# Performance work log

Hardware: AMD Instinct MI355X
Metric: run time of the kernel (lower is better)

The kernel has to match this reference:

```python
import jax, jax.numpy as jnp
import numpy as np

B, S, D = 2, 2048, 1024
H, DH, DM = 16, 64, 4096
EPS = 1e-5
IGNORE = -100000.0


def setup_inputs() -> dict:
    key = jax.random.key(0)
    ks = jax.random.split(key, 14)
    s = 0.02
    return {
        "x": jax.random.normal(ks[0], (B, S, D), jnp.float32),
        "W_Q": jax.random.normal(ks[1], (H, DH, D), jnp.float32) * s,
        "W_K": jax.random.normal(ks[2], (H, DH, D), jnp.float32) * s,
        "W_V": jax.random.normal(ks[3], (H, DH, D), jnp.float32) * s,
        "W_O": jax.random.normal(ks[4], (H, D, DH), jnp.float32) * s,
        "b_Q": jax.random.normal(ks[5], (H, DH), jnp.float32) * s,
        "b_K": jax.random.normal(ks[6], (H, DH), jnp.float32) * s,
        "b_V": jax.random.normal(ks[7], (H, DH), jnp.float32) * s,
        "b_O": jax.random.normal(ks[8], (D,), jnp.float32) * s,
        "W_in": jax.random.normal(ks[9], (DM, D), jnp.float32) * s,
        "b_in": jax.random.normal(ks[10], (DM,), jnp.float32) * s,
        "W_out": jax.random.normal(ks[11], (D, DM), jnp.float32) * s,
        "b_out": jax.random.normal(ks[12], (D,), jnp.float32) * s,
    }


def ln_pre(x):
    x = x - jnp.mean(x, axis=-1, keepdims=True)
    scale = jnp.sqrt(jnp.mean(x * x, axis=-1, keepdims=True) + EPS)
    return x / scale


def gelu_new(x):
    c = np.sqrt(2.0 / np.pi).astype(np.float32)
    return 0.5 * x * (1.0 + jnp.tanh(c * (x + 0.044715 * x ** 3)))


def reference(x, W_Q, W_K, W_V, W_O, b_Q, b_K, b_V, b_O, W_in, b_in, W_out, b_out):
    resid_pre = x
    xn = ln_pre(resid_pre)
    # q,k,v: [B, S, H, DH]
    q = jnp.einsum('ihm,bpm->bpih', W_Q, xn) + b_Q
    k = jnp.einsum('ihm,bpm->bpih', W_K, xn) + b_K
    v = jnp.einsum('ihm,bpm->bpih', W_V, xn) + b_V
    attn_scale = np.sqrt(DH).astype(np.float32)
    # scores: [B, H, Sq, Sk]  (einsum 'bpih,bqih->bipq')
    scores = jnp.einsum('bpih,bqih->bipq', q, k) / attn_scale
    mask = jnp.tril(jnp.ones((S, S), bool))
    scores = jnp.where(mask, scores, IGNORE)
    attn = jax.nn.softmax(scores, axis=-1)
    # z: [B, Sq, H, DH]
    z = jnp.einsum('bpih,biqp->bqih', v, attn)
    attn_out = jnp.einsum('idh,bqih->bqd', W_O, z) + b_O
    resid_mid = resid_pre + attn_out
    m = ln_pre(resid_mid)
    pre = jnp.einsum('md,bpd->bpm', W_in, m) + b_in
    post = gelu_new(pre)
    mlp_out = jnp.einsum('dm,bpm->bpd', W_out, post) + b_out
    return resid_mid + mlp_out
```

## Files before the change

### kernel.cpp

```cpp
#include <hip/hip_runtime.h>

typedef unsigned short u16;
typedef __attribute__((ext_vector_type(8))) short short8;
typedef __attribute__((ext_vector_type(4))) unsigned short ushort4v;
typedef __attribute__((ext_vector_type(4))) float float4v;

__device__ __forceinline__ float bf2f(u16 u) {
  union { unsigned int i; float f; } c; c.i = ((unsigned int)u) << 16; return c.f;
}
__device__ __forceinline__ u16 f2bf(float f) {
  union { float f; unsigned int i; } c; c.f = f;
  unsigned int u = c.i;
  return (u16)((u + 0x7fffu + ((u >> 16) & 1u)) >> 16);
}
__device__ __forceinline__ float gelu_new(float x) {
  const float k1 = 2.30218776f;
  const float k3 = 0.10294233f;
  float x3 = x * x * x;
  float e = __builtin_amdgcn_exp2f(-(k1 * x + k3 * x3));
  return x / (1.0f + e);
}
__device__ __forceinline__ float ldres(const float* p) { return *p; }
__device__ __forceinline__ float ldres(const u16* p) { return bf2f(*p); }

__device__ __forceinline__ void gload_lds16(const u16* g, u16* l) {
  __builtin_amdgcn_global_load_lds(
      (const __attribute__((address_space(1))) unsigned int*)g,
      (__attribute__((address_space(3))) unsigned int*)l, 16, 0, 0);
}

__global__ void cvt_bf16(const float* __restrict__ src, u16* __restrict__ dst) {
  int t = blockIdx.x * 256 + threadIdx.x;
  float4v a = *(const float4v*)(src + (size_t)t * 8);
  float4v b = *(const float4v*)(src + (size_t)t * 8 + 4);
  short8 o;
#pragma unroll
  for (int j = 0; j < 4; ++j) o[j] = (short)f2bf(a[j]);
#pragma unroll
  for (int j = 0; j < 4; ++j) o[4 + j] = (short)f2bf(b[j]);
  *(short8*)(dst + (size_t)t * 8) = o;
}

__global__ void prep_wo(const float* __restrict__ WO, u16* __restrict__ Wot) {
  int t = blockIdx.x * 256 + threadIdx.x;
  int i = t >> 13;
  int d = (t >> 3) & 1023;
  int h0 = (t & 7) * 8;
  const float* src = WO + (size_t)i * 65536 + d * 64 + h0;
  float4v a = *(const float4v*)(src);
  float4v b = *(const float4v*)(src + 4);
  short8 o;
#pragma unroll
  for (int j = 0; j < 4; ++j) o[j] = (short)f2bf(a[j]);
#pragma unroll
  for (int j = 0; j < 4; ++j) o[4 + j] = (short)f2bf(b[j]);
  *(short8*)(Wot + (size_t)d * 1024 + i * 64 + h0) = o;
}

__global__ void prep_bqkv(const float* __restrict__ bQ, const float* __restrict__ bK,
                          const float* __restrict__ bV, float* __restrict__ bqkv) {
  int t = blockIdx.x * 256 + threadIdx.x;
  if (t < 3072)
    bqkv[t] = (t < 1024) ? bQ[t] : (t < 2048) ? bK[t - 1024] : bV[t - 2048];
}

__global__ void ln_f32(const float* __restrict__ x, u16* __restrict__ y) {
  __shared__ float red1[4];
  __shared__ float red2[4];
  int token = blockIdx.x;
  int tid = threadIdx.x;
  int w = tid >> 6;
  const float* xr = x + (size_t)token * 1024;
  float4v v = *(const float4v*)(xr + tid * 4);
  float s = v[0] + v[1] + v[2] + v[3];
#pragma unroll
  for (int m = 32; m >= 1; m >>= 1) s += __shfl_xor(s, m);
  if ((tid & 63) == 0) red1[w] = s;
  __syncthreads();
  float mean = (red1[0] + red1[1] + red1[2] + red1[3]) * (1.0f / 1024.0f);
  float ss = 0.0f;
#pragma unroll
  for (int j = 0; j < 4; ++j) { v[j] -= mean; ss += v[j] * v[j]; }
#pragma unroll
  for (int m = 32; m >= 1; m >>= 1) ss += __shfl_xor(ss, m);
  if ((tid & 63) == 0) red2[w] = ss;
  __syncthreads();
  float ms = (red2[0] + red2[1] + red2[2] + red2[3]) * (1.0f / 1024.0f);
  float inv = 1.0f / sqrtf(ms + 1e-5f);
  ushort4v o;
#pragma unroll
  for (int j = 0; j < 4; ++j) o[j] = f2bf(v[j] * inv);
  *(ushort4v*)(y + (size_t)token * 1024 + tid * 4) = o;
}

template <int BN, int BK, bool GELU, bool VSPLIT, bool DBUF, typename TO, typename TR>
__global__ __launch_bounds__(256) void gemm_bt(
    const u16* __restrict__ A, const u16* __restrict__ Bw,
    const float* __restrict__ bias, const TR* __restrict__ resid,
    TO* __restrict__ C, u16* __restrict__ vTout, int M, int N, int K,
    int lda, int ldc) {
  constexpr int BM = 128;
  constexpr int SEGS = BK / 8;
  constexpr int SMASK = SEGS - 1;
  constexpr int FI = 4, FJ = BN / 32;
  constexpr int CA = BM * SEGS / 256;
  constexpr int CB = BN * SEGS / 256;
  constexpr int NB = DBUF ? 2 : 1;
  __shared__ __align__(16) u16 As[NB][BM * BK];
  __shared__ __align__(16) u16 Bs[NB][BN * BK];
  const int tid = threadIdx.x;
  const int w = tid >> 6, lane = tid & 63;
  const int quad = lane >> 4, l16 = lane & 15;
  const int m0 = blockIdx.x * BM, n0 = blockIdx.y * BN;
  const int wm = (w >> 1) * 64, wn = (w & 1) * (BN / 2);
  const int rmask = l16 & SMASK;
  float4v acc[FI][FJ] = {};

  auto stage = [&](int buf, int k0) {
#pragma unroll
    for (int t = 0; t < CA; ++t) {
      int chunk = (w * CA + t) * 64 + lane;
      int row = chunk / SEGS, seg = chunk % SEGS;
      int sseg = seg ^ (row & SMASK);
      gload_lds16(A + (size_t)(m0 + row) * lda + k0 + sseg * 8,
                  As[buf] + (w * CA + t) * 512);
    }
#pragma unroll
    for (int t = 0; t < CB; ++t) {
      int chunk = (w * CB + t) * 64 + lane;
      int row = chunk / SEGS, seg = chunk % SEGS;
      int sseg = seg ^ (row & SMASK);
      gload_lds16(Bw + (size_t)(n0 + row) * K + k0 + sseg * 8,
                  Bs[buf] + (w * CB + t) * 512);
    }
  };
  auto compute = [&](int buf) {
#pragma unroll
    for (int kk = 0; kk < BK; kk += 32) {
      short8 a[FI], b[FJ];
#pragma unroll
      for (int fi = 0; fi < FI; ++fi)
        a[fi] = *(const short8*)(As[buf] + (wm + fi * 16 + l16) * BK +
                                 ((((kk >> 3) + quad) ^ rmask) << 3));
#pragma unroll
      for (int fj = 0; fj < FJ; ++fj)
        b[fj] = *(const short8*)(Bs[buf] + (wn + fj * 16 + l16) * BK +
                                 ((((kk >> 3) + quad) ^ rmask) << 3));
#pragma unroll
      for (int fi = 0; fi < FI; ++fi)
#pragma unroll
        for (int fj = 0; fj < FJ; ++fj)
          acc[fi][fj] = __builtin_amdgcn_mfma_f32_16x16x32_bf16(
              a[fi], b[fj], acc[fi][fj], 0, 0, 0);
    }
  };

  if constexpr (DBUF) {
    stage(0, 0);
    __syncthreads();
    int cur = 0;
    for (int k0 = 0; k0 < K; k0 += BK) {
      if (k0 + BK < K) stage(cur ^ 1, k0 + BK);
      compute(cur);
      __syncthreads();
      cur ^= 1;
    }
  } else {
    for (int k0 = 0; k0 < K; k0 += BK) {
      __syncthreads();
      stage(0, k0);
      __syncthreads();
      compute(0);
    }
  }

#pragma unroll
  for (int fi = 0; fi < FI; ++fi) {
#pragma unroll
    for (int fj = 0; fj < FJ; ++fj) {
      int col = n0 + wn + fj * 16 + l16;
      float bv = bias ? bias[col] : 0.0f;
#pragma unroll
      for (int r = 0; r < 4; ++r) {
        int row = m0 + wm + fi * 16 + quad * 4 + r;
        float val = acc[fi][fj][r] + bv;
        if (resid) val += ldres(resid + (size_t)row * N + col);
        if (GELU) val = gelu_new(val);
        if (VSPLIT && col >= 2048) {
          vTout[(size_t)(col - 2048) * 4096 + row] = f2bf(val);
        } else if constexpr (sizeof(TO) == 2) {
          C[(size_t)row * ldc + col] = f2bf(val);
        } else {
          C[(size_t)row * ldc + col] = val;
        }
      }
    }
  }
}

__global__ __launch_bounds__(256) void attn_flash(u16* __restrict__ qk,
                                                  const u16* __restrict__ vT) {
  constexpr int PADK = 72;
  constexpr float C2 = 0.18033688011112042f;
  __shared__ __align__(16) u16 Ks[64 * PADK];
  __shared__ __align__(16) u16 Vt[64 * PADK];
  __shared__ __align__(16) u16 Ps[4][16 * PADK];
  const int id = blockIdx.x;
  const int qt = 31 - (id >> 5);
  const int combo = id & 31;
  const int head = combo >> 1, b = combo & 1;
  const int tid = threadIdx.x;
  const int w = tid >> 6, lane = tid & 63;
  const int quad = lane >> 4, l16 = lane & 15;
  const int q0 = qt * 64;
  const size_t tokB = (size_t)b * 2048;

  short8 aq[2];
#pragma unroll
  for (int ks = 0; ks < 2; ++ks)
    aq[ks] = *(const short8*)(qk + (tokB + q0 + w * 16 + l16) * 2048 +
                              head * 64 + ks * 32 + quad * 8);

  const u16* kbase = qk + tokB * 2048 + 1024 + head * 64;
  const u16* vbase = vT + (size_t)head * 64 * 4096 + tokB;

  float m_st[4] = {-1e30f, -1e30f, -1e30f, -1e30f};
  float l_st[4] = {0.f, 0.f, 0.f, 0.f};
  float4v o_acc[4] = {};

  for (int kt = 0; kt <= qt; ++kt) {
    const int kk0 = kt * 64;
    __syncthreads();
#pragma unroll
    for (int i = 0; i < 2; ++i) {
      int flat = tid * 2 + i;
      int row = flat >> 3, seg = flat & 7;
      *(short8*)(Ks + row * PADK + seg * 8) =
          *(const short8*)(kbase + (size_t)(kk0 + row) * 2048 + seg * 8);
      *(short8*)(Vt + row * PADK + seg * 8) =
          *(const short8*)(vbase + (size_t)row * 4096 + kk0 + seg * 8);
    }
    __syncthreads();

    float4v s[4];
#pragma unroll
    for (int fj = 0; fj < 4; ++fj) {
      float4v t = {0.f, 0.f, 0.f, 0.f};
#pragma unroll
      for (int ks = 0; ks < 2; ++ks) {
        short8 bk = *(const short8*)(Ks + (fj * 16 + l16) * PADK + ks * 32 + quad * 8);
        t = __builtin_amdgcn_mfma_f32_16x16x32_bf16(aq[ks], bk, t, 0, 0, 0);
      }
      s[fj] = t;
    }
#pragma unroll
    for (int fj = 0; fj < 4; ++fj)
#pragma unroll
      for (int r = 0; r < 4; ++r) s[fj][r] *= C2;
    if (kt == qt) {
#pragma unroll
      for (int fj = 0; fj < 4; ++fj) {
        int col = kk0 + fj * 16 + l16;
#pragma unroll
        for (int r = 0; r < 4; ++r) {
          int row = q0 + w * 16 + quad * 4 + r;
          if (col > row) s[fj][r] = -1e30f;
        }
      }
    }
    float mx[4];
#pragma unroll
    for (int r = 0; r < 4; ++r) {
      float m = s[0][r];
#pragma unroll
      for (int fj = 1; fj < 4; ++fj) m = fmaxf(m, s[fj][r]);
      m = fmaxf(m, __shfl_xor(m, 1));
      m = fmaxf(m, __shfl_xor(m, 2));
      m = fmaxf(m, __shfl_xor(m, 4));
      m = fmaxf(m, __shfl_xor(m, 8));
      mx[r] = m;
    }
    float alpha[4];
#pragma unroll
    for (int r = 0; r < 4; ++r) {
      float mnew = fmaxf(m_st[r], mx[r]);
      alpha[r] = __builtin_amdgcn_exp2f(m_st[r] - mnew);
      m_st[r] = mnew;
    }
    float rs[4] = {0.f, 0.f, 0.f, 0.f};
#pragma unroll
    for (int fj = 0; fj < 4; ++fj)
#pragma unroll
      for (int r = 0; r < 4; ++r) {
        float pv = __builtin_amdgcn_exp2f(s[fj][r] - m_st[r]);
        s[fj][r] = pv;
        rs[r] += pv;
      }
#pragma unroll
    for (int r = 0; r < 4; ++r) {
      float t = rs[r];
      t += __shfl_xor(t, 1);
      t += __shfl_xor(t, 2);
      t += __shfl_xor(t, 4);
      t += __shfl_xor(t, 8);
      l_st[r] = l_st[r] * alpha[r] + t;
    }
#pragma unroll
    for (int fj = 0; fj < 4; ++fj)
#pragma unroll
      for (int r = 0; r < 4; ++r) o_acc[fj][r] *= alpha[r];
#pragma unroll
    for (int fj = 0; fj < 4; ++fj)
#pragma unroll
      for (int r = 0; r < 4; ++r)
        Ps[w][(quad * 4 + r) * PADK + fj * 16 + l16] = f2bf(s[fj][r]);
    short8 ap[2];
#pragma unroll
    for (int ks = 0; ks < 2; ++ks)
      ap[ks] = *(const short8*)(&Ps[w][l16 * PADK + ks * 32 + quad * 8]);
#pragma unroll
    for (int fj = 0; fj < 4; ++fj)
#pragma unroll
      for (int ks = 0; ks < 2; ++ks) {
        short8 bv = *(const short8*)(Vt + (fj * 16 + l16) * PADK + ks * 32 + quad * 8);
        o_acc[fj] = __builtin_amdgcn_mfma_f32_16x16x32_bf16(ap[ks], bv, o_acc[fj], 0, 0, 0);
      }
  }
#pragma unroll
  for (int r = 0; r < 4; ++r) {
    float inv = 1.0f / l_st[r];
    int row = q0 + w * 16 + quad * 4 + r;
#pragma unroll
    for (int fj = 0; fj < 4; ++fj)
      qk[(tokB + row) * 2048 + head * 64 + fj * 16 + l16] =
          f2bf(o_acc[fj][r] * inv);
  }
}

extern "C" void kernel_launch(void* const* d_in, const int* in_sizes, int n_in,
                              void* d_out, int out_size, void* d_ws, size_t ws_size,
                              hipStream_t stream) {
  const float* x = (const float*)d_in[0];
  const float* W_Q = (const float*)d_in[1];
  const float* W_K = (const float*)d_in[2];
  const float* W_V = (const float*)d_in[3];
  const float* W_O = (const float*)d_in[4];
  const float* b_Q = (const float*)d_in[5];
  const float* b_K = (const float*)d_in[6];
  const float* b_V = (const float*)d_in[7];
  const float* b_O = (const float*)d_in[8];
  const float* W_in = (const float*)d_in[9];
  const float* b_in = (const float*)d_in[10];
  const float* W_out = (const float*)d_in[11];
  const float* b_out = (const float*)d_in[12];
  float* out = (float*)d_out;

  char* ws = (char*)d_ws;
  u16* Wqkv = (u16*)(ws);
  u16* Wot  = (u16*)(ws + 6291456);
  u16* Wib  = (u16*)(ws + 8388608);
  u16* Wob  = (u16*)(ws + 16777216);
  float* bqkv = (float*)(ws + 25165824);
  u16* xn   = (u16*)(ws + 25178112);
  u16* qk   = (u16*)(ws + 33566720);
  u16* vT   = (u16*)(ws + 50343936);
  u16* hbuf = (u16*)(ws + 33566720);
  float* rm = (float*)(ws + 67121152);

  cvt_bf16<<<512, 256, 0, stream>>>(W_Q, Wqkv);
  cvt_bf16<<<512, 256, 0, stream>>>(W_K, Wqkv + 1048576);
  cvt_bf16<<<512, 256, 0, stream>>>(W_V, Wqkv + 2097152);
  cvt_bf16<<<2048, 256, 0, stream>>>(W_in, Wib);
  cvt_bf16<<<2048, 256, 0, stream>>>(W_out, Wob);
  prep_wo<<<512, 256, 0, stream>>>(W_O, Wot);
  prep_bqkv<<<12, 256, 0, stream>>>(b_Q, b_K, b_V, bqkv);

  ln_f32<<<4096, 256, 0, stream>>>(x, xn);
  gemm_bt<128, 64, false, true, false, u16, float><<<dim3(32, 24), 256, 0, stream>>>(
      xn, Wqkv, bqkv, (const float*)nullptr, qk, vT, 4096, 3072, 1024, 1024, 2048);
  attn_flash<<<1024, 256, 0, stream>>>(qk, vT);
  gemm_bt<64, 64, false, false, true, float, float><<<dim3(32, 16), 256, 0, stream>>>(
      qk , Wot, b_O, x, rm, nullptr, 4096, 1024, 1024, 2048, 1024);
  ln_f32<<<4096, 256, 0, stream>>>(rm, xn);
  gemm_bt<128, 64, true, false, false, u16, float><<<dim3(32, 32), 256, 0, stream>>>(
      xn, Wib, b_in, (const float*)nullptr, hbuf, nullptr, 4096, 4096, 1024, 1024, 4096);
  gemm_bt<64, 64, false, false, true, float, float><<<dim3(32, 16), 256, 0, stream>>>(
      hbuf, Wob, b_out, rm, out, nullptr, 4096, 1024, 4096, 4096, 1024);
}
```

Measured before the change: 406.5 us.

## Merge weight conversions, prefetch K/V and cut softmax work in attention

Five weight-conversion launches are merged into one multi-source kernel. The softmax scale is folded into the Q projection epilogue. The attention kernel now prefetches the next K/V tile into registers while computing the current one. It skips the rescale unless the running max grows past a threshold, computes the row sums with an extra MFMA against a ones vector, and packs bf16 conversion with v_cvt_pk_bf16 and s_setprio hints. These cut launch overhead, VALU shuffles and exp work, at the cost of more registers and a lazy-rescale numerical tolerance.

```diff
diff --git a/kernel.cpp b/kernel.cpp
--- a/kernel.cpp
+++ b/kernel.cpp
@@ -12,6 +12,11 @@
   union { float f; unsigned int i; } c; c.f = f;
   unsigned int u = c.i;
   return (u16)((u + 0x7fffu + ((u >> 16) & 1u)) >> 16);
+}
+__device__ __forceinline__ unsigned int cvt_pk_bf16(float a, float b) {
+  unsigned int r;
+  asm("v_cvt_pk_bf16_f32 %0, %1, %2" : "=v"(r) : "v"(a), "v"(b));
+  return r;
 }
 __device__ __forceinline__ float gelu_new(float x) {
   const float k1 = 2.30218776f;
@@ -29,8 +34,19 @@
       (__attribute__((address_space(3))) unsigned int*)l, 16, 0, 0);
 }
 
-__global__ void cvt_bf16(const float* __restrict__ src, u16* __restrict__ dst) {
-  int t = blockIdx.x * 256 + threadIdx.x;
+__global__ void cvt_bf16_multi(const float* __restrict__ s0, const float* __restrict__ s1,
+                               const float* __restrict__ s2, const float* __restrict__ s3,
+                               const float* __restrict__ s4, u16* __restrict__ d0,
+                               u16* __restrict__ d1, u16* __restrict__ d2,
+                               u16* __restrict__ d3, u16* __restrict__ d4) {
+  int bid = blockIdx.x;
+  const float* src; u16* dst; int base;
+  if (bid < 512)       { src = s0; dst = d0; base = 0; }
+  else if (bid < 1024) { src = s1; dst = d1; base = 512; }
+  else if (bid < 1536) { src = s2; dst = d2; base = 1024; }
+  else if (bid < 3584) { src = s3; dst = d3; base = 1536; }
+  else                 { src = s4; dst = d4; base = 3584; }
+  int t = (bid - base) * 256 + threadIdx.x;
   float4v a = *(const float4v*)(src + (size_t)t * 8);
   float4v b = *(const float4v*)(src + (size_t)t * 8 + 4);
   short8 o;
@@ -186,6 +202,7 @@
         float val = acc[fi][fj][r] + bv;
         if (resid) val += ldres(resid + (size_t)row * N + col);
         if (GELU) val = gelu_new(val);
+        if (VSPLIT && col < 1024) val *= 0.18033688011112042f;
         if (VSPLIT && col >= 2048) {
           vTout[(size_t)(col - 2048) * 4096 + row] = f2bf(val);
         } else if constexpr (sizeof(TO) == 2) {
@@ -201,7 +218,7 @@
 __global__ __launch_bounds__(256) void attn_flash(u16* __restrict__ qk,
                                                   const u16* __restrict__ vT) {
   constexpr int PADK = 72;
-  constexpr float C2 = 0.18033688011112042f;
+  constexpr float THR2 = 10.0f;
   __shared__ __align__(16) u16 Ks[64 * PADK];
   __shared__ __align__(16) u16 Vt[64 * PADK];
   __shared__ __align__(16) u16 Ps[4][16 * PADK];
@@ -224,25 +241,47 @@
   const u16* kbase = qk + tokB * 2048 + 1024 + head * 64;
   const u16* vbase = vT + (size_t)head * 64 * 4096 + tokB;
 
+  short8 bones = {};
+  if (l16 == 0) {
+#pragma unroll
+    for (int j = 0; j < 8; ++j) bones[j] = (short)0x3F80;
+  }
+
   float m_st[4] = {-1e30f, -1e30f, -1e30f, -1e30f};
-  float l_st[4] = {0.f, 0.f, 0.f, 0.f};
   float4v o_acc[4] = {};
+  float4v o5 = {0.f, 0.f, 0.f, 0.f};
+
+  const int srow = tid >> 2;
+  const int sseg = (tid & 3) * 2;
+  const u16* kptr = kbase + (size_t)srow * 2048 + sseg * 8;
+  const u16* vptr = vbase + (size_t)srow * 4096 + sseg * 8;
+  u16* ksl = Ks + srow * PADK + sseg * 8;
+  u16* vsl = Vt + srow * PADK + sseg * 8;
+
+  short8 pk0 = *(const short8*)(kptr);
+  short8 pk1 = *(const short8*)(kptr + 8);
+  short8 pv0 = *(const short8*)(vptr);
+  short8 pv1 = *(const short8*)(vptr + 8);
 
   for (int kt = 0; kt <= qt; ++kt) {
     const int kk0 = kt * 64;
     __syncthreads();
-#pragma unroll
-    for (int i = 0; i < 2; ++i) {
-      int flat = tid * 2 + i;
-      int row = flat >> 3, seg = flat & 7;
-      *(short8*)(Ks + row * PADK + seg * 8) =
-          *(const short8*)(kbase + (size_t)(kk0 + row) * 2048 + seg * 8);
-      *(short8*)(Vt + row * PADK + seg * 8) =
-          *(const short8*)(vbase + (size_t)row * 4096 + kk0 + seg * 8);
-    }
+    *(short8*)(ksl) = pk0;
+    *(short8*)(ksl + 8) = pk1;
+    *(short8*)(vsl) = pv0;
+    *(short8*)(vsl + 8) = pv1;
     __syncthreads();
+    if (kt < qt) {
+      const u16* kp = kptr + (size_t)(kk0 + 64) * 2048;
+      const u16* vp = vptr + kk0 + 64;
+      pk0 = *(const short8*)(kp);
+      pk1 = *(const short8*)(kp + 8);
+      pv0 = *(const short8*)(vp);
+      pv1 = *(const short8*)(vp + 8);
+    }
 
     float4v s[4];
+    __builtin_amdgcn_s_setprio(1);
 #pragma unroll
     for (int fj = 0; fj < 4; ++fj) {
       float4v t = {0.f, 0.f, 0.f, 0.f};
@@ -253,10 +292,7 @@
       }
       s[fj] = t;
     }
-#pragma unroll
-    for (int fj = 0; fj < 4; ++fj)
-#pragma unroll
-      for (int r = 0; r < 4; ++r) s[fj][r] *= C2;
+    __builtin_amdgcn_s_setprio(0);
     if (kt == qt) {
 #pragma unroll
       for (int fj = 0; fj < 4; ++fj) {
@@ -271,53 +307,43 @@
     float mx[4];
 #pragma unroll
     for (int r = 0; r < 4; ++r) {
-      float m = s[0][r];
-#pragma unroll
-      for (int fj = 1; fj < 4; ++fj) m = fmaxf(m, s[fj][r]);
+      float m = fmaxf(fmaxf(s[0][r], s[1][r]), fmaxf(s[2][r], s[3][r]));
       m = fmaxf(m, __shfl_xor(m, 1));
       m = fmaxf(m, __shfl_xor(m, 2));
       m = fmaxf(m, __shfl_xor(m, 4));
       m = fmaxf(m, __shfl_xor(m, 8));
       mx[r] = m;
     }
-    float alpha[4];
-#pragma unroll
-    for (int r = 0; r < 4; ++r) {
-      float mnew = fmaxf(m_st[r], mx[r]);
-      alpha[r] = __builtin_amdgcn_exp2f(m_st[r] - mnew);
-      m_st[r] = mnew;
-    }
-    float rs[4] = {0.f, 0.f, 0.f, 0.f};
-#pragma unroll
-    for (int fj = 0; fj < 4; ++fj)
+    bool need = false;
+#pragma unroll
+    for (int r = 0; r < 4; ++r) need |= (mx[r] > m_st[r] + THR2);
+    if (__any(need)) {
 #pragma unroll
       for (int r = 0; r < 4; ++r) {
-        float pv = __builtin_amdgcn_exp2f(s[fj][r] - m_st[r]);
-        s[fj][r] = pv;
-        rs[r] += pv;
-      }
-#pragma unroll
-    for (int r = 0; r < 4; ++r) {
-      float t = rs[r];
-      t += __shfl_xor(t, 1);
-      t += __shfl_xor(t, 2);
-      t += __shfl_xor(t, 4);
-      t += __shfl_xor(t, 8);
-      l_st[r] = l_st[r] * alpha[r] + t;
-    }
-#pragma unroll
-    for (int fj = 0; fj < 4; ++fj)
-#pragma unroll
-      for (int r = 0; r < 4; ++r) o_acc[fj][r] *= alpha[r];
-#pragma unroll
-    for (int fj = 0; fj < 4; ++fj)
-#pragma unroll
-      for (int r = 0; r < 4; ++r)
-        Ps[w][(quad * 4 + r) * PADK + fj * 16 + l16] = f2bf(s[fj][r]);
+        float mnew = fmaxf(m_st[r], mx[r]);
+        float al = __builtin_amdgcn_exp2f(m_st[r] - mnew);
+        m_st[r] = mnew;
+        o5[r] *= al;
+#pragma unroll
+        for (int fj = 0; fj < 4; ++fj) o_acc[fj][r] *= al;
+      }
+    }
+#pragma unroll
+    for (int fj = 0; fj < 4; ++fj) {
+#pragma unroll
+      for (int r = 0; r < 4; r += 2) {
+        float e0 = __builtin_amdgcn_exp2f(s[fj][r] - m_st[r]);
+        float e1 = __builtin_amdgcn_exp2f(s[fj][r + 1] - m_st[r + 1]);
+        unsigned int pp = cvt_pk_bf16(e0, e1);
+        Ps[w][(quad * 4 + r) * PADK + fj * 16 + l16] = (u16)pp;
+        Ps[w][(quad * 4 + r + 1) * PADK + fj * 16 + l16] = (u16)(pp >> 16);
+      }
+    }
     short8 ap[2];
 #pragma unroll
     for (int ks = 0; ks < 2; ++ks)
       ap[ks] = *(const short8*)(&Ps[w][l16 * PADK + ks * 32 + quad * 8]);
+    __builtin_amdgcn_s_setprio(1);
 #pragma unroll
     for (int fj = 0; fj < 4; ++fj)
 #pragma unroll
@@ -325,10 +351,15 @@
         short8 bv = *(const short8*)(Vt + (fj * 16 + l16) * PADK + ks * 32 + quad * 8);
         o_acc[fj] = __builtin_amdgcn_mfma_f32_16x16x32_bf16(ap[ks], bv, o_acc[fj], 0, 0, 0);
       }
+#pragma unroll
+    for (int ks = 0; ks < 2; ++ks)
+      o5 = __builtin_amdgcn_mfma_f32_16x16x32_bf16(ap[ks], bones, o5, 0, 0, 0);
+    __builtin_amdgcn_s_setprio(0);
   }
 #pragma unroll
   for (int r = 0; r < 4; ++r) {
-    float inv = 1.0f / l_st[r];
+    float lsum = __shfl(o5[r], lane & 48);
+    float inv = 1.0f / lsum;
     int row = q0 + w * 16 + quad * 4 + r;
 #pragma unroll
     for (int fj = 0; fj < 4; ++fj)
@@ -367,11 +398,9 @@
   u16* hbuf = (u16*)(ws + 33566720);
   float* rm = (float*)(ws + 67121152);
 
-  cvt_bf16<<<512, 256, 0, stream>>>(W_Q, Wqkv);
-  cvt_bf16<<<512, 256, 0, stream>>>(W_K, Wqkv + 1048576);
-  cvt_bf16<<<512, 256, 0, stream>>>(W_V, Wqkv + 2097152);
-  cvt_bf16<<<2048, 256, 0, stream>>>(W_in, Wib);
-  cvt_bf16<<<2048, 256, 0, stream>>>(W_out, Wob);
+  cvt_bf16_multi<<<5632, 256, 0, stream>>>(W_Q, W_K, W_V, W_in, W_out,
+                                           Wqkv, Wqkv + 1048576, Wqkv + 2097152,
+                                           Wib, Wob);
   prep_wo<<<512, 256, 0, stream>>>(W_O, Wot);
   prep_bqkv<<<12, 256, 0, stream>>>(b_Q, b_K, b_V, bqkv);
 
```

New measurement: 366.5 us. 1.11x faster.
